# Performance work log

Measured on AMD Instinct MI355X. Metric: run time of the kernel, lower is better.

The kernel has to match this reference:

```python
import jax, jax.numpy as jnp
import numpy as np

DT_SCALER = 1.0 / 24.0
EULER_STEPS = 10   # odeint euler, t in [0,1], step_size=0.1
STEP = 0.1


def setup_inputs() -> dict:
    key = jax.random.key(0)
    ks = jax.random.split(key, 10)
    B, T, D, H = 8192, 100, 16, 32
    Hd = min((H + D) * 2, 50)  # 50
    x = jax.random.normal(ks[0], (B, T, D), dtype=jnp.float32)
    dt = jax.random.uniform(ks[1], (B, T, 2), dtype=jnp.float32)
    # dh MLP: Linear(H+D -> Hd), tanh, Linear(Hd -> H), tanh ; init N(0, 0.1), bias 0
    W1 = 0.1 * jax.random.normal(ks[2], (Hd, H + D), dtype=jnp.float32)
    b1 = jnp.zeros((Hd,), jnp.float32)
    W2 = 0.1 * jax.random.normal(ks[3], (H, Hd), dtype=jnp.float32)
    b2 = jnp.zeros((H,), jnp.float32)
    # dy MLP: Linear(H -> 2H), tanh, Linear(2H -> 1)
    W3 = 0.1 * jax.random.normal(ks[4], (2 * H, H), dtype=jnp.float32)
    b3 = jnp.zeros((2 * H,), jnp.float32)
    W4 = 0.1 * jax.random.normal(ks[5], (1, 2 * H), dtype=jnp.float32)
    b4 = jnp.zeros((1,), jnp.float32)
    return {"dt": dt, "x": x, "W1": W1, "b1": b1, "W2": W2, "b2": b2,
            "W3": W3, "b3": b3, "W4": W4, "b4": b4}


def _forward(dt, x, W1, b1, W2, b2, W3, b3, W4, b4):
    B, T, D = x.shape
    H = W2.shape[0]
    dti = (dt[:, :, 1] - dt[:, :, 0])[..., None]  # [B,T,1]
    x_t = jnp.swapaxes(x, 0, 1)      # [T,B,D]
    dt_t = jnp.swapaxes(dti, 0, 1)   # [T,B,1]

    def time_step(h, inp):
        x_i, dt_i = inp              # [B,D], [B,1]
        y = x_i[:, 0:1]              # z0 y-part reset to observation each step
        scale = dt_i * DT_SCALER     # [B,1]

        def euler(carry, _):
            y, h = carry
            dh = jnp.tanh(jnp.tanh(jnp.concatenate([x_i, h], axis=1) @ W1.T + b1) @ W2.T + b2) * scale
            dy = (jnp.tanh(h @ W3.T + b3) @ W4.T + b4) * scale
            return (y + STEP * dy, h + STEP * dh), None

        (y, h), _ = jax.lax.scan(euler, (y, h), None, length=EULER_STEPS)
        return h, y

    h0 = jnp.zeros((B, H), jnp.float32)
    _, mu = jax.lax.scan(time_step, h0, (x_t, dt_t))  # mu: [T,B,1]
    return jnp.swapaxes(mu, 0, 1)                     # [B,T,1]


def reference(dt, x, W1, b1, W2, b2, W3, b3, W4, b4):
    return _forward(dt, x, W1, b1, W2, b2, W3, b3, W4, b4)
```

## Files before the change

kernel.cpp:

```cpp
#include <hip/hip_runtime.h>
#include <stdint.h>

#define T_STEPS 100
#define D_IN 16
#define H_DIM 32
#define HD 50
#define KXH 48
#define EULER 10
#define STEPF 0.1f
#define DT_SCALERF (1.0f/24.0f)
#define TANH_SCALE 2.8853900817779268f

typedef __attribute__((ext_vector_type(8))) short short8;
typedef __attribute__((ext_vector_type(4))) float float4v;
typedef __attribute__((ext_vector_type(4))) uint32_t uint4v;

__device__ __forceinline__ float tanh_pre(float us) {
    float e = __builtin_amdgcn_exp2f(us);
    return 1.0f - 2.0f * __builtin_amdgcn_rcpf(e + 1.0f);
}
__device__ __forceinline__ uint32_t pkbf(float lo, float hi) {
    uint32_t r;
    asm("v_cvt_pk_bf16_f32 %0, %1, %2" : "=v"(r) : "v"(lo), "v"(hi));
    return r;
}
__device__ __forceinline__ short f2bf(float f) {
    uint32_t u = __builtin_bit_cast(uint32_t, f);
    u = u + 0x7fffu + ((u >> 16) & 1u);
    return (short)(u >> 16);
}

__device__ __forceinline__ int zorig(int kk) {
    int f = kk >> 5, q = (kk >> 3) & 3, jj = kk & 7;
    int t = 2 * f + (jj >> 2), r = jj & 3;
    if (t < 3) return t * 16 + q * 4 + r;
    if (r == 0 && q < 2) return 48 + q;
    return -1;
}

__global__ __launch_bounds__(64, 1) void latode_kernel(
    const float* __restrict__ dt, const float* __restrict__ x,
    const float* __restrict__ W1, const float* __restrict__ b1,
    const float* __restrict__ W2, const float* __restrict__ b2,
    const float* __restrict__ W3, const float* __restrict__ b3,
    const float* __restrict__ W4, const float* __restrict__ b4,
    float* __restrict__ out)
{
    const int lane = threadIdx.x & 63;
    const int n16  = lane & 15;
    const int quad = lane >> 4;
    const int b0   = blockIdx.x * 16;

    const float* xrow = x + (size_t)(b0 + n16) * (T_STEPS * D_IN);
    const float* drow = dt + (size_t)(b0 + n16) * (T_STEPS * 2);

    short8 w1h[4], w1x[4], w2f[2][2], w3f[4];
    float4v b3v[4], w4v4[4];

#pragma unroll
    for (int t = 0; t < 4; ++t) {
        int kz = 32 * (t >> 1) + 8 * (n16 >> 2) + 4 * (t & 1) + (n16 & 3);
        int of = zorig(kz);
#pragma unroll
        for (int j = 0; j < 8; ++j) {
            int kk = quad * 8 + j;
            float wh = 0.0f, wx = 0.0f;
            if (of >= 0) {
                wh = W1[of * KXH + 16 + kk];
                if (kk < 16)       wx = W1[of * KXH + kk];
                else if (kk == 16) wx = b1[of];
            }
            w1h[t][j] = f2bf(wh * TANH_SCALE);
            w1x[t][j] = f2bf(wx * TANH_SCALE);
        }
    }
#pragma unroll
    for (int t2 = 0; t2 < 2; ++t2) {
        int hrow = 8 * (n16 >> 2) + 4 * t2 + (n16 & 3);
#pragma unroll
        for (int kt = 0; kt < 2; ++kt)
#pragma unroll
        for (int j = 0; j < 8; ++j) {
            int kk = kt * 32 + quad * 8 + j;
            int oz = zorig(kk);
            float w = 0.0f;
            if (oz >= 0)       w = W2[hrow * HD + oz];
            else if (kk == 63) w = b2[hrow];
            w2f[t2][kt][j] = f2bf(w * TANH_SCALE);
        }
    }
#pragma unroll
    for (int t = 0; t < 4; ++t) {
        int f = t * 16 + n16;
#pragma unroll
        for (int j = 0; j < 8; ++j)
            w3f[t][j] = f2bf(W3[f * H_DIM + quad * 8 + j] * TANH_SCALE);
#pragma unroll
        for (int r = 0; r < 4; ++r) {
            int fr = t * 16 + quad * 4 + r;
            b3v[t][r]  = b3[fr] * TANH_SCALE;
            w4v4[t][r] = W4[fr];
        }
    }
    const float b4s = b4[0];

    const float4v zero4 = {0.f,0.f,0.f,0.f};
    float4v hC0 = zero4, hC1 = zero4;
    short8  hB  = (short8){0,0,0,0,0,0,0,0};
    const uint32_t z1d3 = (quad == 3) ? 0x3f800000u : 0u;

    float4 xa = {0,0,0,0}, xb = {0,0,0,0};
    float2 dtv;
    float y0;
    if (quad < 2) {
        xa = *(const float4*)(xrow + quad * 8);
        xb = *(const float4*)(xrow + quad * 8 + 4);
    }
    dtv = *(const float2*)drow;
    y0  = xrow[0];

#pragma unroll 1
    for (int t = 0; t < T_STEPS; ++t) {
        const float s10 = (dtv.y - dtv.x) * (DT_SCALERF * STEPF);
        const float y0c = y0;
        float psum = 0.f;

        float4v cxa[4];
        {
            uint4v xp = {0,0,0,0};
            if (quad < 2) {
                xp[0] = pkbf(xa.x, xa.y); xp[1] = pkbf(xa.z, xa.w);
                xp[2] = pkbf(xb.x, xb.y); xp[3] = pkbf(xb.z, xb.w);
            } else if (quad == 2) {
                xp[0] = 0x00003f80u;
            }
            short8 xB = __builtin_bit_cast(short8, xp);
#pragma unroll
            for (int tt = 0; tt < 4; ++tt)
                cxa[tt] = __builtin_amdgcn_mfma_f32_16x16x32_bf16(w1x[tt], xB, zero4, 0, 0, 0);
        }

        {
            int tn = (t + 1 < T_STEPS) ? t + 1 : (T_STEPS - 1);
            if (quad < 2) {
                xa = *(const float4*)(xrow + tn * D_IN + quad * 8);
                xb = *(const float4*)(xrow + tn * D_IN + quad * 8 + 4);
            }
            dtv = *(const float2*)(drow + tn * 2);
            y0  = xrow[tn * D_IN];
        }

#pragma unroll 2
        for (int e = 0; e < EULER; ++e) {
            float4v a0 = __builtin_amdgcn_mfma_f32_16x16x32_bf16(w1h[0], hB, cxa[0], 0, 0, 0);
            float4v a1 = __builtin_amdgcn_mfma_f32_16x16x32_bf16(w1h[1], hB, cxa[1], 0, 0, 0);
            float4v a2 = __builtin_amdgcn_mfma_f32_16x16x32_bf16(w1h[2], hB, cxa[2], 0, 0, 0);
            float4v a3 = __builtin_amdgcn_mfma_f32_16x16x32_bf16(w1h[3], hB, cxa[3], 0, 0, 0);
            float4v c0 = __builtin_amdgcn_mfma_f32_16x16x32_bf16(w3f[0], hB, b3v[0], 0, 0, 0);
            float4v c1 = __builtin_amdgcn_mfma_f32_16x16x32_bf16(w3f[1], hB, b3v[1], 0, 0, 0);
            float4v c2 = __builtin_amdgcn_mfma_f32_16x16x32_bf16(w3f[2], hB, b3v[2], 0, 0, 0);
            float4v c3 = __builtin_amdgcn_mfma_f32_16x16x32_bf16(w3f[3], hB, b3v[3], 0, 0, 0);

            uint4v z0, z1;
            z0[0] = pkbf(tanh_pre(a0[0]), tanh_pre(a0[1]));
            z0[1] = pkbf(tanh_pre(a0[2]), tanh_pre(a0[3]));
            z0[2] = pkbf(tanh_pre(a1[0]), tanh_pre(a1[1]));
            z0[3] = pkbf(tanh_pre(a1[2]), tanh_pre(a1[3]));
            z1[0] = pkbf(tanh_pre(a2[0]), tanh_pre(a2[1]));
            z1[1] = pkbf(tanh_pre(a2[2]), tanh_pre(a2[3]));
            z1[2] = pkbf(tanh_pre(a3[0]), 0.0f);
            z1[3] = z1d3;
            short8 zf0 = __builtin_bit_cast(short8, z0);
            short8 zf1 = __builtin_bit_cast(short8, z1);

            float4v u20 = __builtin_amdgcn_mfma_f32_16x16x32_bf16(w2f[0][0], zf0, zero4, 0, 0, 0);
            u20 = __builtin_amdgcn_mfma_f32_16x16x32_bf16(w2f[0][1], zf1, u20, 0, 0, 0);
            float4v u21 = __builtin_amdgcn_mfma_f32_16x16x32_bf16(w2f[1][0], zf0, zero4, 0, 0, 0);
            u21 = __builtin_amdgcn_mfma_f32_16x16x32_bf16(w2f[1][1], zf1, u21, 0, 0, 0);

            float p0 = w4v4[0][0]*tanh_pre(c0[0]) + w4v4[0][1]*tanh_pre(c0[1])
                     + w4v4[0][2]*tanh_pre(c0[2]) + w4v4[0][3]*tanh_pre(c0[3]);
            float p1 = w4v4[1][0]*tanh_pre(c1[0]) + w4v4[1][1]*tanh_pre(c1[1])
                     + w4v4[1][2]*tanh_pre(c1[2]) + w4v4[1][3]*tanh_pre(c1[3]);
            float p2 = w4v4[2][0]*tanh_pre(c2[0]) + w4v4[2][1]*tanh_pre(c2[1])
                     + w4v4[2][2]*tanh_pre(c2[2]) + w4v4[2][3]*tanh_pre(c2[3]);
            float p3 = w4v4[3][0]*tanh_pre(c3[0]) + w4v4[3][1]*tanh_pre(c3[1])
                     + w4v4[3][2]*tanh_pre(c3[2]) + w4v4[3][3]*tanh_pre(c3[3]);
            psum += (p0 + p1) + (p2 + p3);

            hC0[0] += s10 * tanh_pre(u20[0]);
            hC0[1] += s10 * tanh_pre(u20[1]);
            hC0[2] += s10 * tanh_pre(u20[2]);
            hC0[3] += s10 * tanh_pre(u20[3]);
            hC1[0] += s10 * tanh_pre(u21[0]);
            hC1[1] += s10 * tanh_pre(u21[1]);
            hC1[2] += s10 * tanh_pre(u21[2]);
            hC1[3] += s10 * tanh_pre(u21[3]);
            uint4v hp;
            hp[0] = pkbf(hC0[0], hC0[1]); hp[1] = pkbf(hC0[2], hC0[3]);
            hp[2] = pkbf(hC1[0], hC1[1]); hp[3] = pkbf(hC1[2], hC1[3]);
            hB = __builtin_bit_cast(short8, hp);
        }

        float pacc = psum;
        pacc += __shfl_xor(pacc, 16, 64);
        pacc += __shfl_xor(pacc, 32, 64);
        if (lane < 16)
            out[(size_t)(b0 + n16) * T_STEPS + t] = y0c + s10 * (pacc + (float)EULER * b4s);
    }
}

extern "C" void kernel_launch(void* const* d_in, const int* in_sizes, int n_in,
                              void* d_out, int out_size, void* d_ws, size_t ws_size,
                              hipStream_t stream) {
    const float* dt = (const float*)d_in[0];
    const float* x  = (const float*)d_in[1];
    const float* W1 = (const float*)d_in[2];
    const float* b1 = (const float*)d_in[3];
    const float* W2 = (const float*)d_in[4];
    const float* b2 = (const float*)d_in[5];
    const float* W3 = (const float*)d_in[6];
    const float* b3 = (const float*)d_in[7];
    const float* W4 = (const float*)d_in[8];
    const float* b4 = (const float*)d_in[9];
    float* out = (float*)d_out;

    const int B = 8192;
    dim3 grid(B / 16), block(64);
    latode_kernel<<<grid, block, 0, stream>>>(dt, x, W1, b1, W2, b2, W3, b3, W4, b4, out);
}
```

Before: 690.7 us.

## Split dh and dy MLP branches across two waves with LDS hidden-state handoff

Each block now runs two waves. Wave 0 computes the dh MLP and updates h, and wave 1 computes the dy MLP readout from h. Wave 0 publishes the packed h to a double-buffered LDS slot each Euler step, and a barrier follows every step. The aim is to shorten the serial critical path per step and lower register pressure per wave. The cost is a block barrier per Euler iteration plus an LDS round trip, and the dy wave runs one step behind through the double buffer.

```diff
diff --git a/kernel.cpp b/kernel.cpp
--- a/kernel.cpp
+++ b/kernel.cpp
@@ -38,7 +38,7 @@
     return -1;
 }
 
-__global__ __launch_bounds__(64, 1) void latode_kernel(
+__global__ __launch_bounds__(128, 1) void latode_kernel(
     const float* __restrict__ dt, const float* __restrict__ x,
     const float* __restrict__ W1, const float* __restrict__ b1,
     const float* __restrict__ W2, const float* __restrict__ b2,
@@ -46,60 +46,70 @@
     const float* __restrict__ W4, const float* __restrict__ b4,
     float* __restrict__ out)
 {
-    const int lane = threadIdx.x & 63;
+    const int tid  = threadIdx.x;
+    const int wave = tid >> 6;
+    const int lane = tid & 63;
     const int n16  = lane & 15;
     const int quad = lane >> 4;
     const int b0   = blockIdx.x * 16;
 
+    __shared__ __align__(16) uint32_t hslot[2][256];
+
+    for (int i = tid; i < 512; i += 128) ((uint32_t*)hslot)[i] = 0;
+
     const float* xrow = x + (size_t)(b0 + n16) * (T_STEPS * D_IN);
     const float* drow = dt + (size_t)(b0 + n16) * (T_STEPS * 2);
 
-    short8 w1h[4], w1x[4], w2f[2][2], w3f[4];
+    short8 w1h[4], w1x[4], w2f[2][2];
+    short8 w3f[4];
     float4v b3v[4], w4v4[4];
 
-#pragma unroll
-    for (int t = 0; t < 4; ++t) {
-        int kz = 32 * (t >> 1) + 8 * (n16 >> 2) + 4 * (t & 1) + (n16 & 3);
-        int of = zorig(kz);
-#pragma unroll
-        for (int j = 0; j < 8; ++j) {
-            int kk = quad * 8 + j;
-            float wh = 0.0f, wx = 0.0f;
-            if (of >= 0) {
-                wh = W1[of * KXH + 16 + kk];
-                if (kk < 16)       wx = W1[of * KXH + kk];
-                else if (kk == 16) wx = b1[of];
-            }
-            w1h[t][j] = f2bf(wh * TANH_SCALE);
-            w1x[t][j] = f2bf(wx * TANH_SCALE);
-        }
-    }
-#pragma unroll
-    for (int t2 = 0; t2 < 2; ++t2) {
-        int hrow = 8 * (n16 >> 2) + 4 * t2 + (n16 & 3);
-#pragma unroll
-        for (int kt = 0; kt < 2; ++kt)
-#pragma unroll
-        for (int j = 0; j < 8; ++j) {
-            int kk = kt * 32 + quad * 8 + j;
-            int oz = zorig(kk);
-            float w = 0.0f;
-            if (oz >= 0)       w = W2[hrow * HD + oz];
-            else if (kk == 63) w = b2[hrow];
-            w2f[t2][kt][j] = f2bf(w * TANH_SCALE);
-        }
-    }
-#pragma unroll
-    for (int t = 0; t < 4; ++t) {
-        int f = t * 16 + n16;
-#pragma unroll
-        for (int j = 0; j < 8; ++j)
-            w3f[t][j] = f2bf(W3[f * H_DIM + quad * 8 + j] * TANH_SCALE);
-#pragma unroll
-        for (int r = 0; r < 4; ++r) {
-            int fr = t * 16 + quad * 4 + r;
-            b3v[t][r]  = b3[fr] * TANH_SCALE;
-            w4v4[t][r] = W4[fr];
+    if (wave == 0) {
+#pragma unroll
+        for (int t = 0; t < 4; ++t) {
+            int kz = 32 * (t >> 1) + 8 * (n16 >> 2) + 4 * (t & 1) + (n16 & 3);
+            int of = zorig(kz);
+#pragma unroll
+            for (int j = 0; j < 8; ++j) {
+                int kk = quad * 8 + j;
+                float wh = 0.0f, wx = 0.0f;
+                if (of >= 0) {
+                    wh = W1[of * KXH + 16 + kk];
+                    if (kk < 16)       wx = W1[of * KXH + kk];
+                    else if (kk == 16) wx = b1[of];
+                }
+                w1h[t][j] = f2bf(wh * TANH_SCALE);
+                w1x[t][j] = f2bf(wx * TANH_SCALE);
+            }
+        }
+#pragma unroll
+        for (int t2 = 0; t2 < 2; ++t2) {
+            int hrow = 8 * (n16 >> 2) + 4 * t2 + (n16 & 3);
+#pragma unroll
+            for (int kt = 0; kt < 2; ++kt)
+#pragma unroll
+            for (int j = 0; j < 8; ++j) {
+                int kk = kt * 32 + quad * 8 + j;
+                int oz = zorig(kk);
+                float w = 0.0f;
+                if (oz >= 0)       w = W2[hrow * HD + oz];
+                else if (kk == 63) w = b2[hrow];
+                w2f[t2][kt][j] = f2bf(w * TANH_SCALE);
+            }
+        }
+    } else {
+#pragma unroll
+        for (int t = 0; t < 4; ++t) {
+            int f = t * 16 + n16;
+#pragma unroll
+            for (int j = 0; j < 8; ++j)
+                w3f[t][j] = f2bf(W3[f * H_DIM + quad * 8 + j] * TANH_SCALE);
+#pragma unroll
+            for (int r = 0; r < 4; ++r) {
+                int fr = t * 16 + quad * 4 + r;
+                b3v[t][r]  = b3[fr] * TANH_SCALE;
+                w4v4[t][r] = W4[fr];
+            }
         }
     }
     const float b4s = b4[0];
@@ -110,14 +120,20 @@
     const uint32_t z1d3 = (quad == 3) ? 0x3f800000u : 0u;
 
     float4 xa = {0,0,0,0}, xb = {0,0,0,0};
-    float2 dtv;
-    float y0;
-    if (quad < 2) {
-        xa = *(const float4*)(xrow + quad * 8);
-        xb = *(const float4*)(xrow + quad * 8 + 4);
+    float2 dtv = {0.f, 0.f};
+    float y0 = 0.f;
+    if (wave == 0) {
+        if (quad < 2) {
+            xa = *(const float4*)(xrow + quad * 8);
+            xb = *(const float4*)(xrow + quad * 8 + 4);
+        }
+        dtv = *(const float2*)drow;
+    } else {
+        dtv = *(const float2*)drow;
+        y0  = xrow[0];
     }
-    dtv = *(const float2*)drow;
-    y0  = xrow[0];
+
+    __syncthreads();
 
 #pragma unroll 1
     for (int t = 0; t < T_STEPS; ++t) {
@@ -126,7 +142,7 @@
         float psum = 0.f;
 
         float4v cxa[4];
-        {
+        if (wave == 0) {
             uint4v xp = {0,0,0,0};
             if (quad < 2) {
                 xp[0] = pkbf(xa.x, xa.y); xp[1] = pkbf(xa.z, xa.w);
@@ -142,71 +158,82 @@
 
         {
             int tn = (t + 1 < T_STEPS) ? t + 1 : (T_STEPS - 1);
-            if (quad < 2) {
-                xa = *(const float4*)(xrow + tn * D_IN + quad * 8);
-                xb = *(const float4*)(xrow + tn * D_IN + quad * 8 + 4);
-            }
-            dtv = *(const float2*)(drow + tn * 2);
-            y0  = xrow[tn * D_IN];
+            if (wave == 0) {
+                if (quad < 2) {
+                    xa = *(const float4*)(xrow + tn * D_IN + quad * 8);
+                    xb = *(const float4*)(xrow + tn * D_IN + quad * 8 + 4);
+                }
+                dtv = *(const float2*)(drow + tn * 2);
+            } else {
+                dtv = *(const float2*)(drow + tn * 2);
+                y0  = xrow[tn * D_IN];
+            }
         }
 
 #pragma unroll 2
         for (int e = 0; e < EULER; ++e) {
-            float4v a0 = __builtin_amdgcn_mfma_f32_16x16x32_bf16(w1h[0], hB, cxa[0], 0, 0, 0);
-            float4v a1 = __builtin_amdgcn_mfma_f32_16x16x32_bf16(w1h[1], hB, cxa[1], 0, 0, 0);
-            float4v a2 = __builtin_amdgcn_mfma_f32_16x16x32_bf16(w1h[2], hB, cxa[2], 0, 0, 0);
-            float4v a3 = __builtin_amdgcn_mfma_f32_16x16x32_bf16(w1h[3], hB, cxa[3], 0, 0, 0);
-            float4v c0 = __builtin_amdgcn_mfma_f32_16x16x32_bf16(w3f[0], hB, b3v[0], 0, 0, 0);
-            float4v c1 = __builtin_amdgcn_mfma_f32_16x16x32_bf16(w3f[1], hB, b3v[1], 0, 0, 0);
-            float4v c2 = __builtin_amdgcn_mfma_f32_16x16x32_bf16(w3f[2], hB, b3v[2], 0, 0, 0);
-            float4v c3 = __builtin_amdgcn_mfma_f32_16x16x32_bf16(w3f[3], hB, b3v[3], 0, 0, 0);
-
-            uint4v z0, z1;
-            z0[0] = pkbf(tanh_pre(a0[0]), tanh_pre(a0[1]));
-            z0[1] = pkbf(tanh_pre(a0[2]), tanh_pre(a0[3]));
-            z0[2] = pkbf(tanh_pre(a1[0]), tanh_pre(a1[1]));
-            z0[3] = pkbf(tanh_pre(a1[2]), tanh_pre(a1[3]));
-            z1[0] = pkbf(tanh_pre(a2[0]), tanh_pre(a2[1]));
-            z1[1] = pkbf(tanh_pre(a2[2]), tanh_pre(a2[3]));
-            z1[2] = pkbf(tanh_pre(a3[0]), 0.0f);
-            z1[3] = z1d3;
-            short8 zf0 = __builtin_bit_cast(short8, z0);
-            short8 zf1 = __builtin_bit_cast(short8, z1);
-
-            float4v u20 = __builtin_amdgcn_mfma_f32_16x16x32_bf16(w2f[0][0], zf0, zero4, 0, 0, 0);
-            u20 = __builtin_amdgcn_mfma_f32_16x16x32_bf16(w2f[0][1], zf1, u20, 0, 0, 0);
-            float4v u21 = __builtin_amdgcn_mfma_f32_16x16x32_bf16(w2f[1][0], zf0, zero4, 0, 0, 0);
-            u21 = __builtin_amdgcn_mfma_f32_16x16x32_bf16(w2f[1][1], zf1, u21, 0, 0, 0);
-
-            float p0 = w4v4[0][0]*tanh_pre(c0[0]) + w4v4[0][1]*tanh_pre(c0[1])
-                     + w4v4[0][2]*tanh_pre(c0[2]) + w4v4[0][3]*tanh_pre(c0[3]);
-            float p1 = w4v4[1][0]*tanh_pre(c1[0]) + w4v4[1][1]*tanh_pre(c1[1])
-                     + w4v4[1][2]*tanh_pre(c1[2]) + w4v4[1][3]*tanh_pre(c1[3]);
-            float p2 = w4v4[2][0]*tanh_pre(c2[0]) + w4v4[2][1]*tanh_pre(c2[1])
-                     + w4v4[2][2]*tanh_pre(c2[2]) + w4v4[2][3]*tanh_pre(c2[3]);
-            float p3 = w4v4[3][0]*tanh_pre(c3[0]) + w4v4[3][1]*tanh_pre(c3[1])
-                     + w4v4[3][2]*tanh_pre(c3[2]) + w4v4[3][3]*tanh_pre(c3[3]);
-            psum += (p0 + p1) + (p2 + p3);
-
-            hC0[0] += s10 * tanh_pre(u20[0]);
-            hC0[1] += s10 * tanh_pre(u20[1]);
-            hC0[2] += s10 * tanh_pre(u20[2]);
-            hC0[3] += s10 * tanh_pre(u20[3]);
-            hC1[0] += s10 * tanh_pre(u21[0]);
-            hC1[1] += s10 * tanh_pre(u21[1]);
-            hC1[2] += s10 * tanh_pre(u21[2]);
-            hC1[3] += s10 * tanh_pre(u21[3]);
-            uint4v hp;
-            hp[0] = pkbf(hC0[0], hC0[1]); hp[1] = pkbf(hC0[2], hC0[3]);
-            hp[2] = pkbf(hC1[0], hC1[1]); hp[3] = pkbf(hC1[2], hC1[3]);
-            hB = __builtin_bit_cast(short8, hp);
-        }
-
-        float pacc = psum;
-        pacc += __shfl_xor(pacc, 16, 64);
-        pacc += __shfl_xor(pacc, 32, 64);
-        if (lane < 16)
-            out[(size_t)(b0 + n16) * T_STEPS + t] = y0c + s10 * (pacc + (float)EULER * b4s);
+            if (wave == 0) {
+                float4v a0 = __builtin_amdgcn_mfma_f32_16x16x32_bf16(w1h[0], hB, cxa[0], 0, 0, 0);
+                float4v a1 = __builtin_amdgcn_mfma_f32_16x16x32_bf16(w1h[1], hB, cxa[1], 0, 0, 0);
+                float4v a2 = __builtin_amdgcn_mfma_f32_16x16x32_bf16(w1h[2], hB, cxa[2], 0, 0, 0);
+                float4v a3 = __builtin_amdgcn_mfma_f32_16x16x32_bf16(w1h[3], hB, cxa[3], 0, 0, 0);
+                uint4v z0, z1;
+                z0[0] = pkbf(tanh_pre(a0[0]), tanh_pre(a0[1]));
+                z0[1] = pkbf(tanh_pre(a0[2]), tanh_pre(a0[3]));
+                z0[2] = pkbf(tanh_pre(a1[0]), tanh_pre(a1[1]));
+                z0[3] = pkbf(tanh_pre(a1[2]), tanh_pre(a1[3]));
+                z1[0] = pkbf(tanh_pre(a2[0]), tanh_pre(a2[1]));
+                z1[1] = pkbf(tanh_pre(a2[2]), tanh_pre(a2[3]));
+                z1[2] = pkbf(tanh_pre(a3[0]), 0.0f);
+                z1[3] = z1d3;
+                short8 zf0 = __builtin_bit_cast(short8, z0);
+                short8 zf1 = __builtin_bit_cast(short8, z1);
+                float4v u20 = __builtin_amdgcn_mfma_f32_16x16x32_bf16(w2f[0][0], zf0, zero4, 0, 0, 0);
+                u20 = __builtin_amdgcn_mfma_f32_16x16x32_bf16(w2f[0][1], zf1, u20, 0, 0, 0);
+                float4v u21 = __builtin_amdgcn_mfma_f32_16x16x32_bf16(w2f[1][0], zf0, zero4, 0, 0, 0);
+                u21 = __builtin_amdgcn_mfma_f32_16x16x32_bf16(w2f[1][1], zf1, u21, 0, 0, 0);
+                hC0[0] += s10 * tanh_pre(u20[0]);
+                hC0[1] += s10 * tanh_pre(u20[1]);
+                hC0[2] += s10 * tanh_pre(u20[2]);
+                hC0[3] += s10 * tanh_pre(u20[3]);
+                hC1[0] += s10 * tanh_pre(u21[0]);
+                hC1[1] += s10 * tanh_pre(u21[1]);
+                hC1[2] += s10 * tanh_pre(u21[2]);
+                hC1[3] += s10 * tanh_pre(u21[3]);
+                uint4v hp;
+                hp[0] = pkbf(hC0[0], hC0[1]); hp[1] = pkbf(hC0[2], hC0[3]);
+                hp[2] = pkbf(hC1[0], hC1[1]); hp[3] = pkbf(hC1[2], hC1[3]);
+                hB = __builtin_bit_cast(short8, hp);
+                *(uint4v*)&hslot[(e + 1) & 1][lane * 4] = hp;
+            } else {
+                short8 hb = __builtin_bit_cast(short8, *(const uint4v*)&hslot[e & 1][lane * 4]);
+                float4v c0 = __builtin_amdgcn_mfma_f32_16x16x32_bf16(w3f[0], hb, b3v[0], 0, 0, 0);
+                float4v c1 = __builtin_amdgcn_mfma_f32_16x16x32_bf16(w3f[1], hb, b3v[1], 0, 0, 0);
+                float4v c2 = __builtin_amdgcn_mfma_f32_16x16x32_bf16(w3f[2], hb, b3v[2], 0, 0, 0);
+                float4v c3 = __builtin_amdgcn_mfma_f32_16x16x32_bf16(w3f[3], hb, b3v[3], 0, 0, 0);
+                float p0 = w4v4[0][0]*tanh_pre(c0[0]) + w4v4[0][1]*tanh_pre(c0[1])
+                         + w4v4[0][2]*tanh_pre(c0[2]) + w4v4[0][3]*tanh_pre(c0[3]);
+                float p1 = w4v4[1][0]*tanh_pre(c1[0]) + w4v4[1][1]*tanh_pre(c1[1])
+                         + w4v4[1][2]*tanh_pre(c1[2]) + w4v4[1][3]*tanh_pre(c1[3]);
+                float p2 = w4v4[2][0]*tanh_pre(c2[0]) + w4v4[2][1]*tanh_pre(c2[1])
+                         + w4v4[2][2]*tanh_pre(c2[2]) + w4v4[2][3]*tanh_pre(c2[3]);
+                float p3 = w4v4[3][0]*tanh_pre(c3[0]) + w4v4[3][1]*tanh_pre(c3[1])
+                         + w4v4[3][2]*tanh_pre(c3[2]) + w4v4[3][3]*tanh_pre(c3[3]);
+                psum += (p0 + p1) + (p2 + p3);
+            }
+            asm volatile("s_waitcnt lgkmcnt(0)" ::: "memory");
+            __builtin_amdgcn_s_barrier();
+            __builtin_amdgcn_sched_barrier(0);
+        }
+
+        if (wave == 1) {
+            float pacc = psum;
+            pacc += __shfl_xor(pacc, 16, 64);
+            pacc += __shfl_xor(pacc, 32, 64);
+            if (lane < 16)
+                out[(size_t)(b0 + n16) * T_STEPS + t] =
+                    y0c + s10 * (pacc + (float)EULER * b4s);
+        }
     }
 }
 
@@ -226,6 +253,6 @@
     float* out = (float*)d_out;
 
     const int B = 8192;
-    dim3 grid(B / 16), block(64);
+    dim3 grid(B / 16), block(128);
     latode_kernel<<<grid, block, 0, stream>>>(dt, x, W1, b1, W2, b2, W3, b3, W4, b4, out);
 }
```

New measurement: 788.5 us. +14.2%, slower.
